# Kernel tuning notes

Hardware: AMD Instinct MI355X
Metric: run time of the kernel (lower is better)

The kernel has to match this reference:

```python
import jax, jax.numpy as jnp
import numpy as np


def setup_inputs() -> dict:
    key = jax.random.key(0)
    ks = jax.random.split(key, 6)
    B, S, D, H, K = 16384, 16, 256, 128, 32
    s1 = 1.0 / np.sqrt(D)
    s2 = 1.0 / np.sqrt(H)
    s3 = 1.0 / np.sqrt(K)
    return {
        "x": jax.random.normal(ks[0], (B, D), jnp.float32),
        "W1": jax.random.normal(ks[1], (S, D, H), jnp.float32) * s1,
        "b1": jnp.zeros((S, H), jnp.float32),
        "W2": jax.random.normal(ks[2], (S, H, D), jnp.float32) * s2,
        "b2": jnp.zeros((S, D), jnp.float32),
        "Wc1": jax.random.normal(ks[3], (S, D, K), jnp.float32) * s1,
        "bc1": jnp.zeros((S, K), jnp.float32),
        "Wc2": jax.random.normal(ks[4], (S, K), jnp.float32) * s3,
        "bc2": jnp.zeros((S,), jnp.float32),
        "lam": jnp.ones((S,), jnp.float32) / S,  # lambda_weights init = 1/n_sources
    }


def reference(x, W1, b1, W2, b2, Wc1, bc1, Wc2, bc2, lam):
    # Batched per-source 2-layer MLP: [B,D] x [S,D,H] -> [B,S,H]
    h = jax.nn.relu(jnp.einsum("bd,sdh->bsh", x, W1) + b1[None])
    outs = jnp.einsum("bsh,shd->bsd", h, W2) + b2[None]            # [B,S,D]
    # Confidence net on each source output
    ch = jax.nn.relu(jnp.einsum("bsd,sdk->bsk", outs, Wc1) + bc1[None])
    conf = jax.nn.sigmoid(jnp.einsum("bsk,sk->bs", ch, Wc2) + bc2[None])  # [B,S]
    # Weighted, normalized combination
    cw = lam[None, :] * conf                                        # [B,S]
    cw = cw / (cw.sum(axis=1, keepdims=True) + 1e-6)
    out = jnp.einsum("bsd,bs->bd", outs, cw)                        # [B,D]
    return out
```

## Files before the change

### kernel.cpp

```cpp
#include <hip/hip_runtime.h>
#include <math.h>

#define S_N 16
#define D_N 256
#define H_N 128
#define K_N 32
#define BT  64
#define B_N 16384

typedef __attribute__((ext_vector_type(8))) short bf16x8;
typedef __attribute__((ext_vector_type(4))) float f32x4;

#define MFMA(a, b, c) __builtin_amdgcn_mfma_f32_16x16x32_bf16(a, b, c, 0, 0, 0)

static __device__ __forceinline__ unsigned short f2bf(float f) {
  union { float f; unsigned u; } v; v.f = f;
  unsigned r = v.u + 0x7FFFu + ((v.u >> 16) & 1u);
  return (unsigned short)(r >> 16);
}

__global__ __launch_bounds__(256)
void lsi_prep(const float* __restrict__ W1, const float* __restrict__ W2,
              const float* __restrict__ Wc1, const float* __restrict__ b2,
              const float* __restrict__ bc1,
              unsigned short* __restrict__ W1t,
              unsigned short* __restrict__ W2t,
              unsigned short* __restrict__ Wft,
              float* __restrict__ bcf)
{
  const int bid = blockIdx.x;
  if (bid < 1024) {
    __shared__ float t[32][33];
    const float* src; unsigned short* dst; int R, C, r0, c0;
    if (bid < 512) {
      int s = bid >> 5, tt = bid & 31;
      R = 256; C = 128; r0 = (tt >> 2) * 32; c0 = (tt & 3) * 32;
      src = W1 + (size_t)s * 256 * 128; dst = W1t + (size_t)s * 128 * 256;
    } else {
      int s = (bid - 512) >> 5, tt = (bid - 512) & 31;
      R = 128; C = 256; r0 = (tt >> 3) * 32; c0 = (tt & 7) * 32;
      src = W2 + (size_t)s * 128 * 256; dst = W2t + (size_t)s * 256 * 128;
    }
    int li = threadIdx.x >> 5, lj = threadIdx.x & 31;
    #pragma unroll
    for (int i = 0; i < 4; ++i)
      t[li + i * 8][lj] = src[(size_t)(r0 + li + i * 8) * C + c0 + lj];
    __syncthreads();
    #pragma unroll
    for (int i = 0; i < 4; ++i)
      dst[(size_t)(c0 + li + i * 8) * R + r0 + lj] = f2bf(t[lj][li + i * 8]);
    return;
  }
  const int q  = bid - 1024;
  const int s  = q >> 3, hb = q & 7;
  const int t  = threadIdx.x;
  const int hh = hb * 16 + (t >> 4);
  const int kb = (t & 15) * 2;
  const float* w2r = W2 + ((size_t)s * H_N + hh) * D_N;
  const float* wc1 = Wc1 + (size_t)s * D_N * K_N;
  float a0 = 0.f, a1 = 0.f;
  for (int d = 0; d < D_N; ++d) {
    float wv = w2r[d];
    a0 = fmaf(wv, wc1[d * K_N + kb], a0);
    a1 = fmaf(wv, wc1[d * K_N + kb + 1], a1);
  }
  Wft[((size_t)s * K_N + kb) * H_N + hh]     = f2bf(a0);
  Wft[((size_t)s * K_N + kb + 1) * H_N + hh] = f2bf(a1);
  if (hb == 0 && t < K_N) {
    float a = bc1[s * K_N + t];
    for (int d = 0; d < D_N; ++d)
      a = fmaf(b2[s * D_N + d], wc1[d * K_N + t], a);
    bcf[s * K_N + t] = a;
  }
}

__global__ __launch_bounds__(512, 2)
void lsi_main(const float* __restrict__ x,
              const float* __restrict__ b1,
              const float* __restrict__ b2,
              const float* __restrict__ Wc2,
              const float* __restrict__ bc2,
              const float* __restrict__ lam,
              const unsigned short* __restrict__ W1t,
              const unsigned short* __restrict__ W2t,
              const unsigned short* __restrict__ Wft,
              const float* __restrict__ bcf,
              float* __restrict__ out)
{
  __shared__ unsigned short x_lds[BT * D_N];
  __shared__ unsigned short h_lds[2][BT * H_N];
  __shared__ float cw_lds[2][BT];
  __shared__ float wsum_lds[BT];

  const int tid = threadIdx.x;
  const int w   = tid >> 6;
  const int l   = tid & 63;
  const int rA  = l & 15;
  const int g   = l >> 4;
  const int k8  = g * 8;
  const int b0  = blockIdx.x * BT;

  {
    int row = tid >> 3;
    int c0  = (tid & 7) * 32;
    const float* xr = x + (size_t)(b0 + row) * D_N + c0;
    #pragma unroll
    for (int cc = 0; cc < 4; ++cc) {
      float4 f0 = *(const float4*)(xr + cc * 8);
      float4 f1 = *(const float4*)(xr + cc * 8 + 4);
      bf16x8 u;
      u[0] = f2bf(f0.x); u[1] = f2bf(f0.y); u[2] = f2bf(f0.z); u[3] = f2bf(f0.w);
      u[4] = f2bf(f1.x); u[5] = f2bf(f1.y); u[6] = f2bf(f1.z); u[7] = f2bf(f1.w);
      unsigned off = (unsigned)(row * 512 + (c0 + cc * 8) * 2) ^ (unsigned)((row & 7) << 4);
      *(bf16x8*)((char*)x_lds + off) = u;
    }
  }
  if (tid < BT) wsum_lds[tid] = 0.f;

  f32x4 out_acc[2][4];
  f32x4 acc2[2][4];
  #pragma unroll
  for (int a = 0; a < 2; ++a)
    #pragma unroll
    for (int b = 0; b < 4; ++b)
      out_acc[a][b] = (f32x4){0.f, 0.f, 0.f, 0.f};

  auto do_gemm1 = [&](int s, unsigned short* hw) {
    f32x4 acc1[4];
    #pragma unroll
    for (int rt = 0; rt < 4; ++rt) acc1[rt] = (f32x4){0.f, 0.f, 0.f, 0.f};
    const unsigned short* B1 = W1t + ((size_t)s * H_N + w * 16 + rA) * D_N + k8;
    #pragma unroll
    for (int ks = 0; ks < 8; ++ks) {
      bf16x8 bfr = *(const bf16x8*)(B1 + ks * 32);
      #pragma unroll
      for (int rt = 0; rt < 4; ++rt) {
        int row = rt * 16 + rA;
        unsigned off = (unsigned)(row * 512 + (ks * 32 + k8) * 2) ^ (unsigned)((row & 7) << 4);
        bf16x8 afr = *(const bf16x8*)((const char*)x_lds + off);
        acc1[rt] = MFMA(afr, bfr, acc1[rt]);
      }
    }
    const float b1v = b1[s * H_N + w * 16 + rA];
    #pragma unroll
    for (int rt = 0; rt < 4; ++rt)
      #pragma unroll
      for (int i = 0; i < 4; ++i) {
        float v = fmaxf(acc1[rt][i] + b1v, 0.f);
        int row = rt * 16 + g * 4 + i;
        unsigned off = (unsigned)(row * 256 + (w * 16 + rA) * 2) ^ (unsigned)((row & 7) << 4);
        *(unsigned short*)((char*)hw + off) = f2bf(v);
      }
  };

  __syncthreads();
  do_gemm1(0, h_lds[0]);
  __syncthreads();

  for (int s = 0; s < S_N; ++s) {
    const unsigned short* hr = (const unsigned short*)h_lds[s & 1];

    if (s > 0) {
      #pragma unroll
      for (int rt = 0; rt < 4; ++rt) {
        f32x4 c4 = *(const f32x4*)&cw_lds[(s + 1) & 1][rt * 16 + g * 4];
        #pragma unroll
        for (int i = 0; i < 4; ++i) {
          out_acc[0][rt][i] += c4[i] * acc2[0][rt][i];
          out_acc[1][rt][i] += c4[i] * acc2[1][rt][i];
        }
      }
    }

    if (w < 4) {
      f32x4 acc3[2];
      acc3[0] = (f32x4){0.f, 0.f, 0.f, 0.f};
      acc3[1] = (f32x4){0.f, 0.f, 0.f, 0.f};
      const unsigned short* Bf = Wft + ((size_t)s * K_N + rA) * H_N + k8;
      #pragma unroll
      for (int ks = 0; ks < 4; ++ks) {
        int row = w * 16 + rA;
        unsigned off = (unsigned)(row * 256 + (ks * 32 + k8) * 2) ^ (unsigned)((row & 7) << 4);
        bf16x8 afr = *(const bf16x8*)((const char*)hr + off);
        acc3[0] = MFMA(afr, *(const bf16x8*)(Bf + ks * 32), acc3[0]);
        acc3[1] = MFMA(afr, *(const bf16x8*)(Bf + 16 * H_N + ks * 32), acc3[1]);
      }
      const float bcf0 = bcf[s * K_N + rA],  bcf1 = bcf[s * K_N + 16 + rA];
      const float wc20 = Wc2[s * K_N + rA],  wc21 = Wc2[s * K_N + 16 + rA];
      float pz[4];
      #pragma unroll
      for (int i = 0; i < 4; ++i)
        pz[i] = fmaxf(acc3[0][i] + bcf0, 0.f) * wc20 +
                fmaxf(acc3[1][i] + bcf1, 0.f) * wc21;
      #pragma unroll
      for (int m = 1; m < 16; m <<= 1)
        #pragma unroll
        for (int i = 0; i < 4; ++i)
          pz[i] += __shfl_xor(pz[i], m);
      if (rA == 0) {
        const float lam_s = lam[s], bc2_s = bc2[s];
        #pragma unroll
        for (int i = 0; i < 4; ++i) {
          float cv = lam_s / (1.f + __expf(-(pz[i] + bc2_s)));
          cw_lds[s & 1][w * 16 + g * 4 + i] = cv;
          wsum_lds[w * 16 + g * 4 + i] += cv;
        }
      }
    }

    #pragma unroll
    for (int a = 0; a < 2; ++a)
      #pragma unroll
      for (int b = 0; b < 4; ++b)
        acc2[a][b] = (f32x4){0.f, 0.f, 0.f, 0.f};
    {
      const unsigned short* B2 = W2t + ((size_t)s * D_N + w * 32 + rA) * H_N + k8;
      #pragma unroll
      for (int ks = 0; ks < 4; ++ks) {
        bf16x8 afr[4];
        #pragma unroll
        for (int rt = 0; rt < 4; ++rt) {
          int row = rt * 16 + rA;
          unsigned off = (unsigned)(row * 256 + (ks * 32 + k8) * 2) ^ (unsigned)((row & 7) << 4);
          afr[rt] = *(const bf16x8*)((const char*)hr + off);
        }
        #pragma unroll
        for (int ct = 0; ct < 2; ++ct) {
          bf16x8 bfr = *(const bf16x8*)(B2 + ct * 16 * H_N + ks * 32);
          #pragma unroll
          for (int rt = 0; rt < 4; ++rt)
            acc2[ct][rt] = MFMA(afr[rt], bfr, acc2[ct][rt]);
        }
      }
      float b2v0 = b2[s * D_N + w * 32 + rA];
      float b2v1 = b2[s * D_N + w * 32 + 16 + rA];
      #pragma unroll
      for (int rt = 0; rt < 4; ++rt)
        #pragma unroll
        for (int i = 0; i < 4; ++i) {
          acc2[0][rt][i] += b2v0;
          acc2[1][rt][i] += b2v1;
        }
    }

    if (s + 1 < S_N) do_gemm1(s + 1, h_lds[(s + 1) & 1]);

    __syncthreads();
  }

  #pragma unroll
  for (int rt = 0; rt < 4; ++rt) {
    f32x4 c4 = *(const f32x4*)&cw_lds[(S_N - 1) & 1][rt * 16 + g * 4];
    #pragma unroll
    for (int i = 0; i < 4; ++i) {
      out_acc[0][rt][i] += c4[i] * acc2[0][rt][i];
      out_acc[1][rt][i] += c4[i] * acc2[1][rt][i];
    }
  }
  #pragma unroll
  for (int rt = 0; rt < 4; ++rt) {
    f32x4 w4 = *(const f32x4*)&wsum_lds[rt * 16 + g * 4];
    #pragma unroll
    for (int i = 0; i < 4; ++i) {
      int row = rt * 16 + g * 4 + i;
      float winv = 1.f / (w4[i] + 1e-6f);
      out[(size_t)(b0 + row) * D_N + w * 32 + rA]      = out_acc[0][rt][i] * winv;
      out[(size_t)(b0 + row) * D_N + w * 32 + 16 + rA] = out_acc[1][rt][i] * winv;
    }
  }
}

extern "C" void kernel_launch(void* const* d_in, const int* in_sizes, int n_in,
                              void* d_out, int out_size, void* d_ws, size_t ws_size,
                              hipStream_t stream) {
  const float* x   = (const float*)d_in[0];
  const float* W1  = (const float*)d_in[1];
  const float* b1  = (const float*)d_in[2];
  const float* W2  = (const float*)d_in[3];
  const float* b2  = (const float*)d_in[4];
  const float* Wc1 = (const float*)d_in[5];
  const float* bc1 = (const float*)d_in[6];
  const float* Wc2 = (const float*)d_in[7];
  const float* bc2 = (const float*)d_in[8];
  const float* lam = (const float*)d_in[9];
  float* out = (float*)d_out;

  unsigned short* W1t = (unsigned short*)d_ws;
  unsigned short* W2t = W1t + (size_t)S_N * H_N * D_N;
  unsigned short* Wft = W2t + (size_t)S_N * D_N * H_N;
  float* bcf = (float*)(Wft + (size_t)S_N * K_N * H_N);

  lsi_prep<<<dim3(1152), dim3(256), 0, stream>>>(W1, W2, Wc1, b2, bc1,
                                                 W1t, W2t, Wft, bcf);
  lsi_main<<<dim3(B_N / BT), dim3(512), 0, stream>>>(x, b1, b2, Wc2, bc2, lam,
                                                     W1t, W2t, Wft, bcf, out);
}
```

Measured before the change: 123.9 us.

## Switch GEMM1 and GEMM2 to 32x32x16 MFMA tiles with wider LDS swizzle

```diff
diff --git a/kernel.cpp b/kernel.cpp
--- a/kernel.cpp
+++ b/kernel.cpp
@@ -10,8 +10,11 @@
 
 typedef __attribute__((ext_vector_type(8))) short bf16x8;
 typedef __attribute__((ext_vector_type(4))) float f32x4;
-
-#define MFMA(a, b, c) __builtin_amdgcn_mfma_f32_16x16x32_bf16(a, b, c, 0, 0, 0)
+typedef __attribute__((ext_vector_type(16))) float f32x16;
+
+#define MFMA16(a, b, c) __builtin_amdgcn_mfma_f32_16x16x32_bf16(a, b, c, 0, 0, 0)
+#define MFMA32(a, b, c) __builtin_amdgcn_mfma_f32_32x32x16_bf16(a, b, c, 0, 0, 0)
+#define SWZ(r) ((unsigned)(((r) & 15) << 4))
 
 static __device__ __forceinline__ unsigned short f2bf(float f) {
   union { float f; unsigned u; } v; v.f = f;
@@ -95,6 +98,8 @@
   const int tid = threadIdx.x;
   const int w   = tid >> 6;
   const int l   = tid & 63;
+  const int l31 = l & 31;
+  const int hi  = l >> 5;
   const int rA  = l & 15;
   const int g   = l >> 4;
   const int k8  = g * 8;
@@ -111,46 +116,40 @@
       bf16x8 u;
       u[0] = f2bf(f0.x); u[1] = f2bf(f0.y); u[2] = f2bf(f0.z); u[3] = f2bf(f0.w);
       u[4] = f2bf(f1.x); u[5] = f2bf(f1.y); u[6] = f2bf(f1.z); u[7] = f2bf(f1.w);
-      unsigned off = (unsigned)(row * 512 + (c0 + cc * 8) * 2) ^ (unsigned)((row & 7) << 4);
+      unsigned off = (unsigned)(row * 512 + (c0 + cc * 8) * 2) ^ SWZ(row);
       *(bf16x8*)((char*)x_lds + off) = u;
     }
   }
   if (tid < BT) wsum_lds[tid] = 0.f;
 
-  f32x4 out_acc[2][4];
-  f32x4 acc2[2][4];
+  f32x16 out_acc[2];
+  f32x16 acc2[2];
   #pragma unroll
-  for (int a = 0; a < 2; ++a)
-    #pragma unroll
-    for (int b = 0; b < 4; ++b)
-      out_acc[a][b] = (f32x4){0.f, 0.f, 0.f, 0.f};
+  for (int i = 0; i < 16; ++i) { out_acc[0][i] = 0.f; out_acc[1][i] = 0.f; }
 
   auto do_gemm1 = [&](int s, unsigned short* hw) {
-    f32x4 acc1[4];
-    #pragma unroll
-    for (int rt = 0; rt < 4; ++rt) acc1[rt] = (f32x4){0.f, 0.f, 0.f, 0.f};
-    const unsigned short* B1 = W1t + ((size_t)s * H_N + w * 16 + rA) * D_N + k8;
-    #pragma unroll
-    for (int ks = 0; ks < 8; ++ks) {
-      bf16x8 bfr = *(const bf16x8*)(B1 + ks * 32);
-      #pragma unroll
-      for (int rt = 0; rt < 4; ++rt) {
-        int row = rt * 16 + rA;
-        unsigned off = (unsigned)(row * 512 + (ks * 32 + k8) * 2) ^ (unsigned)((row & 7) << 4);
-        bf16x8 afr = *(const bf16x8*)((const char*)x_lds + off);
-        acc1[rt] = MFMA(afr, bfr, acc1[rt]);
-      }
-    }
-    const float b1v = b1[s * H_N + w * 16 + rA];
-    #pragma unroll
-    for (int rt = 0; rt < 4; ++rt)
-      #pragma unroll
-      for (int i = 0; i < 4; ++i) {
-        float v = fmaxf(acc1[rt][i] + b1v, 0.f);
-        int row = rt * 16 + g * 4 + i;
-        unsigned off = (unsigned)(row * 256 + (w * 16 + rA) * 2) ^ (unsigned)((row & 7) << 4);
-        *(unsigned short*)((char*)hw + off) = f2bf(v);
-      }
+    const int rt1 = w >> 2, ct1 = w & 3;
+    const int arow = rt1 * 32 + l31;
+    const int hcol = ct1 * 32 + l31;
+    f32x16 acc1;
+    #pragma unroll
+    for (int i = 0; i < 16; ++i) acc1[i] = 0.f;
+    const unsigned short* B1 = W1t + ((size_t)s * H_N + hcol) * D_N + hi * 8;
+    #pragma unroll
+    for (int kf = 0; kf < 16; ++kf) {
+      bf16x8 bfr = *(const bf16x8*)(B1 + kf * 16);
+      unsigned off = (unsigned)(arow * 512 + kf * 32 + hi * 16) ^ SWZ(arow);
+      bf16x8 afr = *(const bf16x8*)((const char*)x_lds + off);
+      acc1 = MFMA32(afr, bfr, acc1);
+    }
+    const float b1v = b1[s * H_N + hcol];
+    #pragma unroll
+    for (int r = 0; r < 16; ++r) {
+      int row = rt1 * 32 + (r & 3) + 8 * (r >> 2) + 4 * hi;
+      float v = fmaxf(acc1[r] + b1v, 0.f);
+      unsigned off = (unsigned)(row * 256 + hcol * 2) ^ SWZ(row);
+      *(unsigned short*)((char*)hw + off) = f2bf(v);
+    }
   };
 
   __syncthreads();
@@ -162,14 +161,14 @@
 
     if (s > 0) {
       #pragma unroll
-      for (int rt = 0; rt < 4; ++rt) {
-        f32x4 c4 = *(const f32x4*)&cw_lds[(s + 1) & 1][rt * 16 + g * 4];
-        #pragma unroll
-        for (int i = 0; i < 4; ++i) {
-          out_acc[0][rt][i] += c4[i] * acc2[0][rt][i];
-          out_acc[1][rt][i] += c4[i] * acc2[1][rt][i];
-        }
-      }
+      for (int rt = 0; rt < 2; ++rt)
+        #pragma unroll
+        for (int q = 0; q < 4; ++q) {
+          f32x4 c4 = *(const f32x4*)&cw_lds[(s + 1) & 1][rt * 32 + q * 8 + hi * 4];
+          #pragma unroll
+          for (int i = 0; i < 4; ++i)
+            out_acc[rt][q * 4 + i] += c4[i] * acc2[rt][q * 4 + i];
+        }
     }
 
     if (w < 4) {
@@ -180,10 +179,10 @@
       #pragma unroll
       for (int ks = 0; ks < 4; ++ks) {
         int row = w * 16 + rA;
-        unsigned off = (unsigned)(row * 256 + (ks * 32 + k8) * 2) ^ (unsigned)((row & 7) << 4);
+        unsigned off = (unsigned)(row * 256 + (ks * 32 + k8) * 2) ^ SWZ(row);
         bf16x8 afr = *(const bf16x8*)((const char*)hr + off);
-        acc3[0] = MFMA(afr, *(const bf16x8*)(Bf + ks * 32), acc3[0]);
-        acc3[1] = MFMA(afr, *(const bf16x8*)(Bf + 16 * H_N + ks * 32), acc3[1]);
+        acc3[0] = MFMA16(afr, *(const bf16x8*)(Bf + ks * 32), acc3[0]);
+        acc3[1] = MFMA16(afr, *(const bf16x8*)(Bf + 16 * H_N + ks * 32), acc3[1]);
       }
       const float bcf0 = bcf[s * K_N + rA],  bcf1 = bcf[s * K_N + 16 + rA];
       const float wc20 = Wc2[s * K_N + rA],  wc21 = Wc2[s * K_N + 16 + rA];
@@ -209,64 +208,57 @@
     }
 
     #pragma unroll
-    for (int a = 0; a < 2; ++a)
-      #pragma unroll
-      for (int b = 0; b < 4; ++b)
-        acc2[a][b] = (f32x4){0.f, 0.f, 0.f, 0.f};
+    for (int i = 0; i < 16; ++i) { acc2[0][i] = 0.f; acc2[1][i] = 0.f; }
     {
-      const unsigned short* B2 = W2t + ((size_t)s * D_N + w * 32 + rA) * H_N + k8;
-      #pragma unroll
-      for (int ks = 0; ks < 4; ++ks) {
-        bf16x8 afr[4];
-        #pragma unroll
-        for (int rt = 0; rt < 4; ++rt) {
-          int row = rt * 16 + rA;
-          unsigned off = (unsigned)(row * 256 + (ks * 32 + k8) * 2) ^ (unsigned)((row & 7) << 4);
-          afr[rt] = *(const bf16x8*)((const char*)hr + off);
-        }
-        #pragma unroll
-        for (int ct = 0; ct < 2; ++ct) {
-          bf16x8 bfr = *(const bf16x8*)(B2 + ct * 16 * H_N + ks * 32);
-          #pragma unroll
-          for (int rt = 0; rt < 4; ++rt)
-            acc2[ct][rt] = MFMA(afr[rt], bfr, acc2[ct][rt]);
-        }
-      }
-      float b2v0 = b2[s * D_N + w * 32 + rA];
-      float b2v1 = b2[s * D_N + w * 32 + 16 + rA];
-      #pragma unroll
-      for (int rt = 0; rt < 4; ++rt)
+      const int dcol = w * 32 + l31;
+      const unsigned short* B2 = W2t + ((size_t)s * D_N + dcol) * H_N + hi * 8;
+      #pragma unroll
+      for (int kf = 0; kf < 8; ++kf) {
+        bf16x8 bfr = *(const bf16x8*)(B2 + kf * 16);
+        #pragma unroll
+        for (int rt = 0; rt < 2; ++rt) {
+          int arow = rt * 32 + l31;
+          unsigned off = (unsigned)(arow * 256 + kf * 32 + hi * 16) ^ SWZ(arow);
+          bf16x8 afr = *(const bf16x8*)((const char*)hr + off);
+          acc2[rt] = MFMA32(afr, bfr, acc2[rt]);
+        }
+      }
+      const float b2v = b2[s * D_N + dcol];
+      #pragma unroll
+      for (int rt = 0; rt < 2; ++rt)
+        #pragma unroll
+        for (int r = 0; r < 16; ++r)
+          acc2[rt][r] += b2v;
+    }
+
+    if (s + 1 < S_N) do_gemm1(s + 1, h_lds[(s + 1) & 1]);
+
+    __syncthreads();
+  }
+
+  #pragma unroll
+  for (int rt = 0; rt < 2; ++rt)
+    #pragma unroll
+    for (int q = 0; q < 4; ++q) {
+      f32x4 c4 = *(const f32x4*)&cw_lds[(S_N - 1) & 1][rt * 32 + q * 8 + hi * 4];
+      #pragma unroll
+      for (int i = 0; i < 4; ++i)
+        out_acc[rt][q * 4 + i] += c4[i] * acc2[rt][q * 4 + i];
+    }
+  {
+    const int dcol = w * 32 + l31;
+    #pragma unroll
+    for (int rt = 0; rt < 2; ++rt)
+      #pragma unroll
+      for (int q = 0; q < 4; ++q) {
+        f32x4 w4 = *(const f32x4*)&wsum_lds[rt * 32 + q * 8 + hi * 4];
         #pragma unroll
         for (int i = 0; i < 4; ++i) {
-          acc2[0][rt][i] += b2v0;
-          acc2[1][rt][i] += b2v1;
-        }
-    }
-
-    if (s + 1 < S_N) do_gemm1(s + 1, h_lds[(s + 1) & 1]);
-
-    __syncthreads();
-  }
-
-  #pragma unroll
-  for (int rt = 0; rt < 4; ++rt) {
-    f32x4 c4 = *(const f32x4*)&cw_lds[(S_N - 1) & 1][rt * 16 + g * 4];
-    #pragma unroll
-    for (int i = 0; i < 4; ++i) {
-      out_acc[0][rt][i] += c4[i] * acc2[0][rt][i];
-      out_acc[1][rt][i] += c4[i] * acc2[1][rt][i];
-    }
-  }
-  #pragma unroll
-  for (int rt = 0; rt < 4; ++rt) {
-    f32x4 w4 = *(const f32x4*)&wsum_lds[rt * 16 + g * 4];
-    #pragma unroll
-    for (int i = 0; i < 4; ++i) {
-      int row = rt * 16 + g * 4 + i;
-      float winv = 1.f / (w4[i] + 1e-6f);
-      out[(size_t)(b0 + row) * D_N + w * 32 + rA]      = out_acc[0][rt][i] * winv;
-      out[(size_t)(b0 + row) * D_N + w * 32 + 16 + rA] = out_acc[1][rt][i] * winv;
-    }
+          int row = rt * 32 + q * 8 + hi * 4 + i;
+          float winv = 1.f / (w4[i] + 1e-6f);
+          out[(size_t)(b0 + row) * D_N + dcol] = out_acc[rt][q * 4 + i] * winv;
+        }
+      }
   }
 }
 
```

Measured after the change: 136.4 us. +10.1%, slower.

## Split fused kernel into stage1/normalize/stage2 passes through a global H buffer

Applied to the files above, without the earlier changes.

```diff
diff --git a/kernel.cpp b/kernel.cpp
--- a/kernel.cpp
+++ b/kernel.cpp
@@ -5,13 +5,16 @@
 #define D_N 256
 #define H_N 128
 #define K_N 32
-#define BT  64
 #define B_N 16384
 
 typedef __attribute__((ext_vector_type(8))) short bf16x8;
 typedef __attribute__((ext_vector_type(4))) float f32x4;
-
-#define MFMA(a, b, c) __builtin_amdgcn_mfma_f32_16x16x32_bf16(a, b, c, 0, 0, 0)
+typedef __attribute__((ext_vector_type(16))) float f32x16;
+
+#define MFMA16(a, b, c) __builtin_amdgcn_mfma_f32_16x16x32_bf16(a, b, c, 0, 0, 0)
+#define MFMA32(a, b, c) __builtin_amdgcn_mfma_f32_32x32x16_bf16(a, b, c, 0, 0, 0)
+#define SWZ(r)  ((unsigned)(((r) & 15) << 4))
+#define SWZ8(r) ((unsigned)(((r) & 7) << 4))
 
 static __device__ __forceinline__ unsigned short f2bf(float f) {
   union { float f; unsigned u; } v; v.f = f;
@@ -74,23 +77,201 @@
   }
 }
 
+__global__ __launch_bounds__(256)
+void lsi_stage1(const float* __restrict__ x, const float* __restrict__ b1,
+                const unsigned short* __restrict__ W1t,
+                const unsigned short* __restrict__ Wft,
+                const float* __restrict__ bcf, const float* __restrict__ Wc2,
+                unsigned short* __restrict__ H, float* __restrict__ z_t)
+{
+  __shared__ unsigned short x_lds[32 * D_N];
+  __shared__ unsigned short h_lds[32 * H_N];
+
+  const int p   = blockIdx.x;
+  const int s   = (p >> 3) & 15;
+  const int rg  = (p & 7) + 8 * (p >> 7);
+  const int b0  = rg * 32;
+
+  const int tid = threadIdx.x;
+  const int w   = tid >> 6;
+  const int l   = tid & 63;
+  const int l31 = l & 31;
+  const int hi  = l >> 5;
+  const int rA  = l & 15;
+  const int g   = l >> 4;
+
+  {
+    int row = tid >> 3;
+    int c0  = (tid & 7) * 32;
+    const float* xr = x + (size_t)(b0 + row) * D_N + c0;
+    #pragma unroll
+    for (int cc = 0; cc < 4; ++cc) {
+      float4 f0 = *(const float4*)(xr + cc * 8);
+      float4 f1 = *(const float4*)(xr + cc * 8 + 4);
+      bf16x8 u;
+      u[0] = f2bf(f0.x); u[1] = f2bf(f0.y); u[2] = f2bf(f0.z); u[3] = f2bf(f0.w);
+      u[4] = f2bf(f1.x); u[5] = f2bf(f1.y); u[6] = f2bf(f1.z); u[7] = f2bf(f1.w);
+      unsigned off = (unsigned)(row * 512 + (c0 + cc * 8) * 2) ^ SWZ(row);
+      *(bf16x8*)((char*)x_lds + off) = u;
+    }
+  }
+  __syncthreads();
+
+  {
+    const int hcol = w * 32 + l31;
+    f32x16 acc1;
+    #pragma unroll
+    for (int i = 0; i < 16; ++i) acc1[i] = 0.f;
+    const unsigned short* B1 = W1t + ((size_t)s * H_N + hcol) * D_N + hi * 8;
+    #pragma unroll
+    for (int kf = 0; kf < 16; ++kf) {
+      bf16x8 bfr = *(const bf16x8*)(B1 + kf * 16);
+      unsigned off = (unsigned)(l31 * 512 + kf * 32 + hi * 16) ^ SWZ(l31);
+      bf16x8 afr = *(const bf16x8*)((const char*)x_lds + off);
+      acc1 = MFMA32(afr, bfr, acc1);
+    }
+    const float b1v = b1[s * H_N + hcol];
+    #pragma unroll
+    for (int r = 0; r < 16; ++r) {
+      int row = (r & 3) + 8 * (r >> 2) + 4 * hi;
+      float v = fmaxf(acc1[r] + b1v, 0.f);
+      unsigned off = (unsigned)(row * 256 + hcol * 2) ^ SWZ(row);
+      *(unsigned short*)((char*)h_lds + off) = f2bf(v);
+    }
+  }
+  __syncthreads();
+
+  if (w < 2) {
+    f32x4 acc3[2];
+    acc3[0] = (f32x4){0.f, 0.f, 0.f, 0.f};
+    acc3[1] = (f32x4){0.f, 0.f, 0.f, 0.f};
+    const unsigned short* Bf = Wft + ((size_t)s * K_N + rA) * H_N + g * 8;
+    #pragma unroll
+    for (int ks = 0; ks < 4; ++ks) {
+      int row = w * 16 + rA;
+      unsigned off = (unsigned)(row * 256 + (ks * 32 + g * 8) * 2) ^ SWZ(row);
+      bf16x8 afr = *(const bf16x8*)((const char*)h_lds + off);
+      acc3[0] = MFMA16(afr, *(const bf16x8*)(Bf + ks * 32), acc3[0]);
+      acc3[1] = MFMA16(afr, *(const bf16x8*)(Bf + 16 * H_N + ks * 32), acc3[1]);
+    }
+    const float bcf0 = bcf[s * K_N + rA],  bcf1 = bcf[s * K_N + 16 + rA];
+    const float wc20 = Wc2[s * K_N + rA],  wc21 = Wc2[s * K_N + 16 + rA];
+    float pz[4];
+    #pragma unroll
+    for (int i = 0; i < 4; ++i)
+      pz[i] = fmaxf(acc3[0][i] + bcf0, 0.f) * wc20 +
+              fmaxf(acc3[1][i] + bcf1, 0.f) * wc21;
+    #pragma unroll
+    for (int m = 1; m < 16; m <<= 1)
+      #pragma unroll
+      for (int i = 0; i < 4; ++i)
+        pz[i] += __shfl_xor(pz[i], m);
+    if (rA == 0) {
+      #pragma unroll
+      for (int i = 0; i < 4; ++i)
+        z_t[(size_t)s * B_N + b0 + w * 16 + g * 4 + i] = pz[i];
+    }
+  } else {
+    const int u = tid - 128;
+    unsigned short* Hs = H + (size_t)s * B_N * H_N;
+    #pragma unroll
+    for (int i = 0; i < 4; ++i) {
+      int c   = u + 128 * i;
+      int row = c >> 4;
+      int cc  = c & 15;
+      unsigned off = (unsigned)(row * 256 + cc * 16) ^ SWZ(row);
+      bf16x8 v = *(const bf16x8*)((const char*)h_lds + off);
+      *(bf16x8*)(Hs + (size_t)(b0 + row) * H_N + cc * 8) = v;
+    }
+  }
+}
+
+__global__ __launch_bounds__(256)
+void lsi_norm(const float* __restrict__ z_t, const float* __restrict__ lam,
+              const float* __restrict__ bc2, float* __restrict__ w_t)
+{
+  const int b = blockIdx.x * 256 + threadIdx.x;
+  float cv[S_N];
+  float sum = 0.f;
+  #pragma unroll
+  for (int s = 0; s < S_N; ++s) {
+    float c = lam[s] / (1.f + __expf(-(z_t[(size_t)s * B_N + b] + bc2[s])));
+    cv[s] = c;
+    sum += c;
+  }
+  const float winv = 1.f / (sum + 1e-6f);
+  #pragma unroll
+  for (int s = 0; s < S_N; ++s)
+    w_t[(size_t)s * B_N + b] = cv[s] * winv;
+}
+
+__global__ __launch_bounds__(256)
+void lsi_stage2(const unsigned short* __restrict__ H,
+                const unsigned short* __restrict__ W2t,
+                const float* __restrict__ b2, const float* __restrict__ w_t,
+                float* __restrict__ out)
+{
+  const int b0  = blockIdx.x * 32;
+  const int tid = threadIdx.x;
+  const int w   = tid >> 6;
+  const int l   = tid & 63;
+  const int l31 = l & 31;
+  const int hi  = l >> 5;
+  const int dc0 = w * 64 + l31;
+  const int dc1 = dc0 + 32;
+
+  f32x16 oa0, oa1;
+  #pragma unroll
+  for (int i = 0; i < 16; ++i) { oa0[i] = 0.f; oa1[i] = 0.f; }
+
+  for (int s = 0; s < S_N; ++s) {
+    const unsigned short* Hs  = H + ((size_t)s * B_N + b0 + l31) * H_N + hi * 8;
+    const unsigned short* B2a = W2t + ((size_t)s * D_N + dc0) * H_N + hi * 8;
+    const unsigned short* B2b = W2t + ((size_t)s * D_N + dc1) * H_N + hi * 8;
+    f32x16 t0, t1;
+    #pragma unroll
+    for (int i = 0; i < 16; ++i) { t0[i] = 0.f; t1[i] = 0.f; }
+    #pragma unroll
+    for (int kf = 0; kf < 8; ++kf) {
+      bf16x8 afr = *(const bf16x8*)(Hs + kf * 16);
+      t0 = MFMA32(afr, *(const bf16x8*)(B2a + kf * 16), t0);
+      t1 = MFMA32(afr, *(const bf16x8*)(B2b + kf * 16), t1);
+    }
+    const float b20 = b2[s * D_N + dc0];
+    const float b21 = b2[s * D_N + dc1];
+    #pragma unroll
+    for (int q = 0; q < 4; ++q) {
+      f32x4 w4 = *(const f32x4*)(w_t + (size_t)s * B_N + b0 + q * 8 + hi * 4);
+      #pragma unroll
+      for (int i = 0; i < 4; ++i) {
+        oa0[q * 4 + i] += w4[i] * (t0[q * 4 + i] + b20);
+        oa1[q * 4 + i] += w4[i] * (t1[q * 4 + i] + b21);
+      }
+    }
+  }
+  #pragma unroll
+  for (int q = 0; q < 4; ++q)
+    #pragma unroll
+    for (int i = 0; i < 4; ++i) {
+      int row = q * 8 + hi * 4 + i;
+      out[(size_t)(b0 + row) * D_N + dc0] = oa0[q * 4 + i];
+      out[(size_t)(b0 + row) * D_N + dc1] = oa1[q * 4 + i];
+    }
+}
+
 __global__ __launch_bounds__(512, 2)
-void lsi_main(const float* __restrict__ x,
-              const float* __restrict__ b1,
-              const float* __restrict__ b2,
-              const float* __restrict__ Wc2,
-              const float* __restrict__ bc2,
-              const float* __restrict__ lam,
+void lsi_mono(const float* __restrict__ x, const float* __restrict__ b1,
+              const float* __restrict__ b2, const float* __restrict__ Wc2,
+              const float* __restrict__ bc2, const float* __restrict__ lam,
               const unsigned short* __restrict__ W1t,
               const unsigned short* __restrict__ W2t,
               const unsigned short* __restrict__ Wft,
-              const float* __restrict__ bcf,
-              float* __restrict__ out)
+              const float* __restrict__ bcf, float* __restrict__ out)
 {
-  __shared__ unsigned short x_lds[BT * D_N];
-  __shared__ unsigned short h_lds[2][BT * H_N];
-  __shared__ float cw_lds[2][BT];
-  __shared__ float wsum_lds[BT];
+  __shared__ unsigned short x_lds[64 * D_N];
+  __shared__ unsigned short h_lds[2][64 * H_N];
+  __shared__ float cw_lds[2][64];
+  __shared__ float wsum_lds[64];
 
   const int tid = threadIdx.x;
   const int w   = tid >> 6;
@@ -98,7 +279,7 @@
   const int rA  = l & 15;
   const int g   = l >> 4;
   const int k8  = g * 8;
-  const int b0  = blockIdx.x * BT;
+  const int b0  = blockIdx.x * 64;
 
   {
     int row = tid >> 3;
@@ -111,11 +292,11 @@
       bf16x8 u;
       u[0] = f2bf(f0.x); u[1] = f2bf(f0.y); u[2] = f2bf(f0.z); u[3] = f2bf(f0.w);
       u[4] = f2bf(f1.x); u[5] = f2bf(f1.y); u[6] = f2bf(f1.z); u[7] = f2bf(f1.w);
-      unsigned off = (unsigned)(row * 512 + (c0 + cc * 8) * 2) ^ (unsigned)((row & 7) << 4);
+      unsigned off = (unsigned)(row * 512 + (c0 + cc * 8) * 2) ^ SWZ8(row);
       *(bf16x8*)((char*)x_lds + off) = u;
     }
   }
-  if (tid < BT) wsum_lds[tid] = 0.f;
+  if (tid < 64) wsum_lds[tid] = 0.f;
 
   f32x4 out_acc[2][4];
   f32x4 acc2[2][4];
@@ -136,9 +317,9 @@
       #pragma unroll
       for (int rt = 0; rt < 4; ++rt) {
         int row = rt * 16 + rA;
-        unsigned off = (unsigned)(row * 512 + (ks * 32 + k8) * 2) ^ (unsigned)((row & 7) << 4);
+        unsigned off = (unsigned)(row * 512 + (ks * 32 + k8) * 2) ^ SWZ8(row);
         bf16x8 afr = *(const bf16x8*)((const char*)x_lds + off);
-        acc1[rt] = MFMA(afr, bfr, acc1[rt]);
+        acc1[rt] = MFMA16(afr, bfr, acc1[rt]);
       }
     }
     const float b1v = b1[s * H_N + w * 16 + rA];
@@ -148,7 +329,7 @@
       for (int i = 0; i < 4; ++i) {
         float v = fmaxf(acc1[rt][i] + b1v, 0.f);
         int row = rt * 16 + g * 4 + i;
-        unsigned off = (unsigned)(row * 256 + (w * 16 + rA) * 2) ^ (unsigned)((row & 7) << 4);
+        unsigned off = (unsigned)(row * 256 + (w * 16 + rA) * 2) ^ SWZ8(row);
         *(unsigned short*)((char*)hw + off) = f2bf(v);
       }
   };
@@ -159,7 +340,6 @@
 
   for (int s = 0; s < S_N; ++s) {
     const unsigned short* hr = (const unsigned short*)h_lds[s & 1];
-
     if (s > 0) {
       #pragma unroll
       for (int rt = 0; rt < 4; ++rt) {
@@ -171,7 +351,6 @@
         }
       }
     }
-
     if (w < 4) {
       f32x4 acc3[2];
       acc3[0] = (f32x4){0.f, 0.f, 0.f, 0.f};
@@ -180,10 +359,10 @@
       #pragma unroll
       for (int ks = 0; ks < 4; ++ks) {
         int row = w * 16 + rA;
-        unsigned off = (unsigned)(row * 256 + (ks * 32 + k8) * 2) ^ (unsigned)((row & 7) << 4);
+        unsigned off = (unsigned)(row * 256 + (ks * 32 + k8) * 2) ^ SWZ8(row);
         bf16x8 afr = *(const bf16x8*)((const char*)hr + off);
-        acc3[0] = MFMA(afr, *(const bf16x8*)(Bf + ks * 32), acc3[0]);
-        acc3[1] = MFMA(afr, *(const bf16x8*)(Bf + 16 * H_N + ks * 32), acc3[1]);
+        acc3[0] = MFMA16(afr, *(const bf16x8*)(Bf + ks * 32), acc3[0]);
+        acc3[1] = MFMA16(afr, *(const bf16x8*)(Bf + 16 * H_N + ks * 32), acc3[1]);
       }
       const float bcf0 = bcf[s * K_N + rA],  bcf1 = bcf[s * K_N + 16 + rA];
       const float wc20 = Wc2[s * K_N + rA],  wc21 = Wc2[s * K_N + 16 + rA];
@@ -207,7 +386,6 @@
         }
       }
     }
-
     #pragma unroll
     for (int a = 0; a < 2; ++a)
       #pragma unroll
@@ -221,7 +399,7 @@
         #pragma unroll
         for (int rt = 0; rt < 4; ++rt) {
           int row = rt * 16 + rA;
-          unsigned off = (unsigned)(row * 256 + (ks * 32 + k8) * 2) ^ (unsigned)((row & 7) << 4);
+          unsigned off = (unsigned)(row * 256 + (ks * 32 + k8) * 2) ^ SWZ8(row);
           afr[rt] = *(const bf16x8*)((const char*)hr + off);
         }
         #pragma unroll
@@ -229,7 +407,7 @@
           bf16x8 bfr = *(const bf16x8*)(B2 + ct * 16 * H_N + ks * 32);
           #pragma unroll
           for (int rt = 0; rt < 4; ++rt)
-            acc2[ct][rt] = MFMA(afr[rt], bfr, acc2[ct][rt]);
+            acc2[ct][rt] = MFMA16(afr[rt], bfr, acc2[ct][rt]);
         }
       }
       float b2v0 = b2[s * D_N + w * 32 + rA];
@@ -242,9 +420,7 @@
           acc2[1][rt][i] += b2v1;
         }
     }
-
     if (s + 1 < S_N) do_gemm1(s + 1, h_lds[(s + 1) & 1]);
-
     __syncthreads();
   }
 
@@ -289,9 +465,20 @@
   unsigned short* W2t = W1t + (size_t)S_N * H_N * D_N;
   unsigned short* Wft = W2t + (size_t)S_N * D_N * H_N;
   float* bcf = (float*)(Wft + (size_t)S_N * K_N * H_N);
+  float* z_t = bcf + S_N * K_N;
+  float* w_t = z_t + (size_t)S_N * B_N;
+  unsigned short* H = (unsigned short*)(w_t + (size_t)S_N * B_N);
+  size_t need = (size_t)((char*)(H + (size_t)S_N * B_N * H_N) - (char*)d_ws);
 
   lsi_prep<<<dim3(1152), dim3(256), 0, stream>>>(W1, W2, Wc1, b2, bc1,
                                                  W1t, W2t, Wft, bcf);
-  lsi_main<<<dim3(B_N / BT), dim3(512), 0, stream>>>(x, b1, b2, Wc2, bc2, lam,
-                                                     W1t, W2t, Wft, bcf, out);
-}
+  if (ws_size >= need) {
+    lsi_stage1<<<dim3(8192), dim3(256), 0, stream>>>(x, b1, W1t, Wft, bcf, Wc2,
+                                                     H, z_t);
+    lsi_norm<<<dim3(B_N / 256), dim3(256), 0, stream>>>(z_t, lam, bc2, w_t);
+    lsi_stage2<<<dim3(B_N / 32), dim3(256), 0, stream>>>(H, W2t, b2, w_t, out);
+  } else {
+    lsi_mono<<<dim3(B_N / 64), dim3(512), 0, stream>>>(x, b1, b2, Wc2, bc2, lam,
+                                                       W1t, W2t, Wft, bcf, out);
+  }
+}
```

Result: slower. 224.1 us (+80.9%).

## Double workgroup to 1024 threads and split MFMA tiles across sixteen waves

Applied to the files above, without the earlier changes.

```diff
diff --git a/kernel.cpp b/kernel.cpp
--- a/kernel.cpp
+++ b/kernel.cpp
@@ -11,7 +11,8 @@
 typedef __attribute__((ext_vector_type(8))) short bf16x8;
 typedef __attribute__((ext_vector_type(4))) float f32x4;
 
-#define MFMA(a, b, c) __builtin_amdgcn_mfma_f32_16x16x32_bf16(a, b, c, 0, 0, 0)
+#define MFMA16(a, b, c) __builtin_amdgcn_mfma_f32_16x16x32_bf16(a, b, c, 0, 0, 0)
+#define SWZ8(r) ((unsigned)(((r) & 7) << 4))
 
 static __device__ __forceinline__ unsigned short f2bf(float f) {
   union { float f; unsigned u; } v; v.f = f;
@@ -74,7 +75,7 @@
   }
 }
 
-__global__ __launch_bounds__(512, 2)
+__global__ __launch_bounds__(1024)
 void lsi_main(const float* __restrict__ x,
               const float* __restrict__ b1,
               const float* __restrict__ b2,
@@ -87,8 +88,8 @@
               const float* __restrict__ bcf,
               float* __restrict__ out)
 {
-  __shared__ unsigned short x_lds[BT * D_N];
-  __shared__ unsigned short h_lds[2][BT * H_N];
+  __shared__ __align__(16) unsigned short x_lds[BT * D_N];
+  __shared__ __align__(16) unsigned short h_lds[2][BT * H_N];
   __shared__ float cw_lds[2][BT];
   __shared__ float wsum_lds[BT];
 
@@ -99,56 +100,56 @@
   const int g   = l >> 4;
   const int k8  = g * 8;
   const int b0  = blockIdx.x * BT;
+  const int ct1 = w & 7;
+  const int rh  = w >> 3;
 
   {
-    int row = tid >> 3;
-    int c0  = (tid & 7) * 32;
+    int row = tid >> 4;
+    int c0  = (tid & 15) * 16;
     const float* xr = x + (size_t)(b0 + row) * D_N + c0;
     #pragma unroll
-    for (int cc = 0; cc < 4; ++cc) {
+    for (int cc = 0; cc < 2; ++cc) {
       float4 f0 = *(const float4*)(xr + cc * 8);
       float4 f1 = *(const float4*)(xr + cc * 8 + 4);
       bf16x8 u;
       u[0] = f2bf(f0.x); u[1] = f2bf(f0.y); u[2] = f2bf(f0.z); u[3] = f2bf(f0.w);
       u[4] = f2bf(f1.x); u[5] = f2bf(f1.y); u[6] = f2bf(f1.z); u[7] = f2bf(f1.w);
-      unsigned off = (unsigned)(row * 512 + (c0 + cc * 8) * 2) ^ (unsigned)((row & 7) << 4);
+      unsigned off = (unsigned)(row * 512 + (c0 + cc * 8) * 2) ^ SWZ8(row);
       *(bf16x8*)((char*)x_lds + off) = u;
     }
   }
   if (tid < BT) wsum_lds[tid] = 0.f;
 
-  f32x4 out_acc[2][4];
-  f32x4 acc2[2][4];
+  f32x4 out_acc[4];
+  f32x4 acc2[4];
   #pragma unroll
-  for (int a = 0; a < 2; ++a)
-    #pragma unroll
-    for (int b = 0; b < 4; ++b)
-      out_acc[a][b] = (f32x4){0.f, 0.f, 0.f, 0.f};
+  for (int rt = 0; rt < 4; ++rt)
+    out_acc[rt] = (f32x4){0.f, 0.f, 0.f, 0.f};
 
   auto do_gemm1 = [&](int s, unsigned short* hw) {
-    f32x4 acc1[4];
-    #pragma unroll
-    for (int rt = 0; rt < 4; ++rt) acc1[rt] = (f32x4){0.f, 0.f, 0.f, 0.f};
-    const unsigned short* B1 = W1t + ((size_t)s * H_N + w * 16 + rA) * D_N + k8;
+    f32x4 acc1[2];
+    acc1[0] = (f32x4){0.f, 0.f, 0.f, 0.f};
+    acc1[1] = (f32x4){0.f, 0.f, 0.f, 0.f};
+    const unsigned short* B1 = W1t + ((size_t)s * H_N + ct1 * 16 + rA) * D_N + k8;
     #pragma unroll
     for (int ks = 0; ks < 8; ++ks) {
       bf16x8 bfr = *(const bf16x8*)(B1 + ks * 32);
       #pragma unroll
-      for (int rt = 0; rt < 4; ++rt) {
-        int row = rt * 16 + rA;
-        unsigned off = (unsigned)(row * 512 + (ks * 32 + k8) * 2) ^ (unsigned)((row & 7) << 4);
+      for (int rt = 0; rt < 2; ++rt) {
+        int row = rh * 32 + rt * 16 + rA;
+        unsigned off = (unsigned)(row * 512 + (ks * 32 + k8) * 2) ^ SWZ8(row);
         bf16x8 afr = *(const bf16x8*)((const char*)x_lds + off);
-        acc1[rt] = MFMA(afr, bfr, acc1[rt]);
-      }
-    }
-    const float b1v = b1[s * H_N + w * 16 + rA];
-    #pragma unroll
-    for (int rt = 0; rt < 4; ++rt)
+        acc1[rt] = MFMA16(afr, bfr, acc1[rt]);
+      }
+    }
+    const float b1v = b1[s * H_N + ct1 * 16 + rA];
+    #pragma unroll
+    for (int rt = 0; rt < 2; ++rt)
       #pragma unroll
       for (int i = 0; i < 4; ++i) {
         float v = fmaxf(acc1[rt][i] + b1v, 0.f);
-        int row = rt * 16 + g * 4 + i;
-        unsigned off = (unsigned)(row * 256 + (w * 16 + rA) * 2) ^ (unsigned)((row & 7) << 4);
+        int row = rh * 32 + rt * 16 + g * 4 + i;
+        unsigned off = (unsigned)(row * 256 + (ct1 * 16 + rA) * 2) ^ SWZ8(row);
         *(unsigned short*)((char*)hw + off) = f2bf(v);
       }
   };
@@ -165,10 +166,8 @@
       for (int rt = 0; rt < 4; ++rt) {
         f32x4 c4 = *(const f32x4*)&cw_lds[(s + 1) & 1][rt * 16 + g * 4];
         #pragma unroll
-        for (int i = 0; i < 4; ++i) {
-          out_acc[0][rt][i] += c4[i] * acc2[0][rt][i];
-          out_acc[1][rt][i] += c4[i] * acc2[1][rt][i];
-        }
+        for (int i = 0; i < 4; ++i)
+          out_acc[rt][i] += c4[i] * acc2[rt][i];
       }
     }
 
@@ -180,10 +179,10 @@
       #pragma unroll
       for (int ks = 0; ks < 4; ++ks) {
         int row = w * 16 + rA;
-        unsigned off = (unsigned)(row * 256 + (ks * 32 + k8) * 2) ^ (unsigned)((row & 7) << 4);
+        unsigned off = (unsigned)(row * 256 + (ks * 32 + k8) * 2) ^ SWZ8(row);
         bf16x8 afr = *(const bf16x8*)((const char*)hr + off);
-        acc3[0] = MFMA(afr, *(const bf16x8*)(Bf + ks * 32), acc3[0]);
-        acc3[1] = MFMA(afr, *(const bf16x8*)(Bf + 16 * H_N + ks * 32), acc3[1]);
+        acc3[0] = MFMA16(afr, *(const bf16x8*)(Bf + ks * 32), acc3[0]);
+        acc3[1] = MFMA16(afr, *(const bf16x8*)(Bf + 16 * H_N + ks * 32), acc3[1]);
       }
       const float bcf0 = bcf[s * K_N + rA],  bcf1 = bcf[s * K_N + 16 + rA];
       const float wc20 = Wc2[s * K_N + rA],  wc21 = Wc2[s * K_N + 16 + rA];
@@ -209,38 +208,27 @@
     }
 
     #pragma unroll
-    for (int a = 0; a < 2; ++a)
-      #pragma unroll
-      for (int b = 0; b < 4; ++b)
-        acc2[a][b] = (f32x4){0.f, 0.f, 0.f, 0.f};
+    for (int rt = 0; rt < 4; ++rt)
+      acc2[rt] = (f32x4){0.f, 0.f, 0.f, 0.f};
     {
-      const unsigned short* B2 = W2t + ((size_t)s * D_N + w * 32 + rA) * H_N + k8;
+      const unsigned short* B2 = W2t + ((size_t)s * D_N + w * 16 + rA) * H_N + k8;
       #pragma unroll
       for (int ks = 0; ks < 4; ++ks) {
-        bf16x8 afr[4];
+        bf16x8 bfr = *(const bf16x8*)(B2 + ks * 32);
         #pragma unroll
         for (int rt = 0; rt < 4; ++rt) {
           int row = rt * 16 + rA;
-          unsigned off = (unsigned)(row * 256 + (ks * 32 + k8) * 2) ^ (unsigned)((row & 7) << 4);
-          afr[rt] = *(const bf16x8*)((const char*)hr + off);
+          unsigned off = (unsigned)(row * 256 + (ks * 32 + k8) * 2) ^ SWZ8(row);
+          bf16x8 afr = *(const bf16x8*)((const char*)hr + off);
+          acc2[rt] = MFMA16(afr, bfr, acc2[rt]);
         }
-        #pragma unroll
-        for (int ct = 0; ct < 2; ++ct) {
-          bf16x8 bfr = *(const bf16x8*)(B2 + ct * 16 * H_N + ks * 32);
-          #pragma unroll
-          for (int rt = 0; rt < 4; ++rt)
-            acc2[ct][rt] = MFMA(afr[rt], bfr, acc2[ct][rt]);
-        }
-      }
-      float b2v0 = b2[s * D_N + w * 32 + rA];
-      float b2v1 = b2[s * D_N + w * 32 + 16 + rA];
+      }
+      const float b2v = b2[s * D_N + w * 16 + rA];
       #pragma unroll
       for (int rt = 0; rt < 4; ++rt)
         #pragma unroll
-        for (int i = 0; i < 4; ++i) {
-          acc2[0][rt][i] += b2v0;
-          acc2[1][rt][i] += b2v1;
-        }
+        for (int i = 0; i < 4; ++i)
+          acc2[rt][i] += b2v;
     }
 
     if (s + 1 < S_N) do_gemm1(s + 1, h_lds[(s + 1) & 1]);
@@ -252,10 +240,8 @@
   for (int rt = 0; rt < 4; ++rt) {
     f32x4 c4 = *(const f32x4*)&cw_lds[(S_N - 1) & 1][rt * 16 + g * 4];
     #pragma unroll
-    for (int i = 0; i < 4; ++i) {
-      out_acc[0][rt][i] += c4[i] * acc2[0][rt][i];
-      out_acc[1][rt][i] += c4[i] * acc2[1][rt][i];
-    }
+    for (int i = 0; i < 4; ++i)
+      out_acc[rt][i] += c4[i] * acc2[rt][i];
   }
   #pragma unroll
   for (int rt = 0; rt < 4; ++rt) {
@@ -264,8 +250,7 @@
     for (int i = 0; i < 4; ++i) {
       int row = rt * 16 + g * 4 + i;
       float winv = 1.f / (w4[i] + 1e-6f);
-      out[(size_t)(b0 + row) * D_N + w * 32 + rA]      = out_acc[0][rt][i] * winv;
-      out[(size_t)(b0 + row) * D_N + w * 32 + 16 + rA] = out_acc[1][rt][i] * winv;
+      out[(size_t)(b0 + row) * D_N + w * 16 + rA] = out_acc[rt][i] * winv;
     }
   }
 }
@@ -292,6 +277,6 @@
 
   lsi_prep<<<dim3(1152), dim3(256), 0, stream>>>(W1, W2, Wc1, b2, bc1,
                                                  W1t, W2t, Wft, bcf);
-  lsi_main<<<dim3(B_N / BT), dim3(512), 0, stream>>>(x, b1, b2, Wc2, bc2, lam,
-                                                     W1t, W2t, Wft, bcf, out);
-}
+  lsi_main<<<dim3(B_N / BT), dim3(1024), 0, stream>>>(x, b1, b2, Wc2, bc2, lam,
+                                                      W1t, W2t, Wft, bcf, out);
+}
```

Measured after the change: 146.6 us. 18.3% more time.
